# Kernel optimization log

Hardware: AMD Instinct MI355X
Metric: run time of the kernel (lower is better)

The kernel has to match this reference:

```python
import jax, jax.numpy as jnp
import numpy as np

B, I, D = 256, 1152, 8   # batch, input_num_capsule, input_dim_vector
C, O = 10, 16            # num_capsule, dim_vector
NUM_ROUTING = 3
EPS = 1e-7


def squash(s, axis=-1):
    # v = ||s||^2 / (1 + ||s||^2) * s / ||s||
    n2 = jnp.sum(jnp.square(s), axis=axis, keepdims=True)
    return (n2 / (1.0 + n2)) * s / jnp.sqrt(n2 + EPS)


def setup_inputs() -> dict:
    key = jax.random.key(0)
    kx, kw = jax.random.split(key)
    x = jax.random.normal(kx, (B, I, D), dtype=jnp.float32)
    W = jax.random.normal(kw, (I, C, D, O), dtype=jnp.float32) * 0.05
    return {"x": x, "W": W}


def reference(x, W):
    # inputs_hat[b,i,c,o] = sum_d x[b,i,d] * W[i,c,d,o]
    # (the original tf.scan over batch of per-sample batch_dots == this einsum)
    inputs_hat = jnp.einsum('bid,icdo->bico', x, W)  # [B,I,C,O]

    bias = jnp.zeros((1, I, C, 1), dtype=x.dtype)    # routing logits
    outputs = None
    for r in range(NUM_ROUTING):
        c = jax.nn.softmax(bias, axis=2)             # softmax over num_capsule
        s = jnp.sum(c[..., None].squeeze(-1) * inputs_hat, axis=1, keepdims=True)  # [B,1,C,O]
        outputs = squash(s, axis=-1)                 # [B,1,C,O]
        if r != NUM_ROUTING - 1:
            bias = bias + jnp.sum(inputs_hat * outputs, axis=-1, keepdims=False)[..., None].squeeze(-1)[..., None]
    return outputs.reshape(B, C, O)
```

## Files before the change

### kernel.cpp

```cpp
#include <hip/hip_runtime.h>
#include <hip/hip_bf16.h>
#include <math.h>


#define B_ 256
#define I_ 1152
#define D_ 8
#define C_ 10
#define O_ 16
#define CO_ (C_*O_)
#define EPS_ 1e-7f

#define IC1 16
#define NIC1 (I_/IC1)
#define BT 16
#define NBT (B_/BT)
#define T1 320
#define IC3 128
#define NIC3 (I_/IC3)
#define T3 320

__global__ __launch_bounds__(T1) void k1_hat(
    const float* __restrict__ x,
    const float* __restrict__ W,
    __hip_bfloat16* __restrict__ hat,
    float* __restrict__ sPart1)
{
    __shared__ float xs[BT * IC1 * D_];
    __shared__ float sred[BT][CO_];
    const int tid = threadIdx.x;
    const int ic = blockIdx.x, bt = blockIdx.y;
    const int i0 = ic * IC1, b0 = bt * BT;

    for (int j = tid; j < BT * IC1 * D_ / 4; j += T1) {
        const int bb = j >> 5, r = j & 31;
        ((float4*)xs)[j] =
            *(const float4*)&x[(((size_t)(b0 + bb)) * I_ + i0) * D_ + r * 4];
    }
    __syncthreads();

    const int ig = tid / 80, r = tid % 80;
    const int c = r / 8, o2 = r % 8;

    float2 acc[BT];
    #pragma unroll
    for (int bb = 0; bb < BT; ++bb) acc[bb] = make_float2(0.0f, 0.0f);

    const float2* W2 = (const float2*)W;

    for (int k = 0; k < IC1 / 4; ++k) {
        const int il = ig * (IC1 / 4) + k;
        const int i = i0 + il;
        float2 wv[D_];
        const float2* wp = W2 + ((size_t)i * C_ + c) * (D_ * O_ / 2) + o2;
        #pragma unroll
        for (int d = 0; d < D_; ++d) wv[d] = wp[d * (O_ / 2)];
        #pragma unroll
        for (int bb = 0; bb < BT; ++bb) {
            const float* xp = &xs[(bb * IC1 + il) * D_];
            float h0 = 0.0f, h1 = 0.0f;
            #pragma unroll
            for (int d = 0; d < D_; ++d) {
                const float xv = xp[d];
                h0 = fmaf(xv, wv[d].x, h0);
                h1 = fmaf(xv, wv[d].y, h1);
            }
            acc[bb].x += h0; acc[bb].y += h1;
            *(__hip_bfloat162*)&hat[((size_t)(b0 + bb) * I_ + i) * CO_ + c * O_ + o2 * 2] =
                __float22bfloat162_rn(make_float2(h0, h1));
        }
    }

    if (ig == 0) {
        #pragma unroll
        for (int bb = 0; bb < BT; ++bb) {
            sred[bb][c * O_ + o2 * 2]     = acc[bb].x;
            sred[bb][c * O_ + o2 * 2 + 1] = acc[bb].y;
        }
    }
    __syncthreads();
    #pragma unroll
    for (int g = 1; g < 4; ++g) {
        if (ig == g) {
            #pragma unroll
            for (int bb = 0; bb < BT; ++bb) {
                sred[bb][c * O_ + o2 * 2]     += acc[bb].x;
                sred[bb][c * O_ + o2 * 2 + 1] += acc[bb].y;
            }
        }
        __syncthreads();
    }
    if (tid < CO_) {
        for (int bb = 0; bb < BT; ++bb)
            sPart1[((size_t)ic * B_ + (b0 + bb)) * CO_ + tid] = sred[bb][tid];
    }
}

__device__ __forceinline__ void route_body(
    const __hip_bfloat16* __restrict__ hat, const float* vr,
    float* __restrict__ sPartR, int ic, int b, int il, int c, int tid)
{
    __shared__ float pb[32][C_];
    __shared__ float sr[32][CO_ + 4];
    const int i0 = ic * IC3;

    float sacc[O_];
    #pragma unroll
    for (int o = 0; o < O_; ++o) sacc[o] = 0.0f;

    for (int sb = 0; sb < IC3 / 32; ++sb) {
        const int i = i0 + sb * 32 + il;
        const uint4* hp = (const uint4*)&hat[((size_t)b * I_ + i) * CO_ + c * O_];
        const uint4 ha = hp[0], hb = hp[1];
        float hf[O_];
        {
            const unsigned u[8] = {ha.x, ha.y, ha.z, ha.w, hb.x, hb.y, hb.z, hb.w};
            #pragma unroll
            for (int q = 0; q < 8; ++q) {
                hf[2 * q]     = __uint_as_float(u[q] << 16);
                hf[2 * q + 1] = __uint_as_float(u[q] & 0xffff0000u);
            }
        }
        float p = 0.0f;
        #pragma unroll
        for (int o = 0; o < O_; ++o) p = fmaf(hf[o], vr[o], p);
        pb[il][c] = p;
        __syncthreads();
        float pv[C_];
        #pragma unroll
        for (int q = 0; q < C_; ++q) pv[q] = pb[il][q];
        float m = pv[0];
        #pragma unroll
        for (int q = 1; q < C_; ++q) m = fmaxf(m, pv[q]);
        float sum = 0.0f;
        #pragma unroll
        for (int q = 0; q < C_; ++q) sum += __expf(pv[q] - m);
        const float route = __expf(p - m) * __builtin_amdgcn_rcpf(sum);
        #pragma unroll
        for (int o = 0; o < O_; ++o) sacc[o] = fmaf(route, hf[o], sacc[o]);
        __syncthreads();
    }

    #pragma unroll
    for (int o = 0; o < O_; ++o) sr[il][c * O_ + o] = sacc[o];
    __syncthreads();
    if (tid < CO_) {
        float s = 0.0f;
        #pragma unroll
        for (int k = 0; k < 32; ++k) s += sr[k][tid];
        sPartR[((size_t)ic * B_ + b) * CO_ + tid] = s;
    }
}

__global__ __launch_bounds__(T3) void k_route2(
    const __hip_bfloat16* __restrict__ hat,
    const float* __restrict__ veff,
    float* __restrict__ sPartR)
{
    const int tid = threadIdx.x;
    const int il = tid / C_, c = tid % C_;
    const int ic = blockIdx.x, b = blockIdx.y;
    float vr[O_];
    #pragma unroll
    for (int o = 0; o < O_; ++o) vr[o] = veff[(size_t)b * CO_ + c * O_ + o];
    route_body(hat, vr, sPartR, ic, b, il, c, tid);
}

__global__ __launch_bounds__(T3) void k_route3(
    const __hip_bfloat16* __restrict__ hat,
    const float* __restrict__ veff1,
    const float* __restrict__ sPartR1,
    float* __restrict__ sPartR2)
{
    __shared__ float veffs[CO_];
    const int tid = threadIdx.x;
    const int il = tid / C_, c = tid % C_;
    const int ic = blockIdx.x, b = blockIdx.y;

    if (tid < CO_) {
        float s = 0.0f;
        #pragma unroll
        for (int k = 0; k < NIC3; ++k)
            s += sPartR1[((size_t)k * B_ + b) * CO_ + tid];
        float n2 = s * s;
        n2 += __shfl_xor(n2, 1);
        n2 += __shfl_xor(n2, 2);
        n2 += __shfl_xor(n2, 4);
        n2 += __shfl_xor(n2, 8);
        const float sc = n2 / ((1.0f + n2) * sqrtf(n2 + EPS_));
        veffs[tid] = veff1[(size_t)b * CO_ + tid] + s * sc;
    }
    __syncthreads();

    float vr[O_];
    #pragma unroll
    for (int o = 0; o < O_; ++o) vr[o] = veffs[c * O_ + o];
    route_body(hat, vr, sPartR2, ic, b, il, c, tid);
}

__global__ __launch_bounds__(640) void k_squash(
    const float* __restrict__ sPart,
    int nchunk, float scale,
    const float* __restrict__ prev,
    float* __restrict__ dst)
{
    __shared__ float red[4][CO_];
    const int b = blockIdx.x, tid = threadIdx.x;
    const int q = tid / CO_;
    const int co = tid % CO_;
    float s = 0.0f;
    for (int k = q; k < nchunk; k += 4)
        s += sPart[((size_t)k * B_ + b) * CO_ + co];
    red[q][co] = s;
    __syncthreads();
    if (tid < CO_) {
        s = (red[0][co] + red[1][co]) + (red[2][co] + red[3][co]);
        s *= scale;
        float n2 = s * s;
        n2 += __shfl_xor(n2, 1);
        n2 += __shfl_xor(n2, 2);
        n2 += __shfl_xor(n2, 4);
        n2 += __shfl_xor(n2, 8);
        const float sc = n2 / ((1.0f + n2) * sqrtf(n2 + EPS_));
        const float v = s * sc;
        dst[(size_t)b * CO_ + co] = (prev ? prev[(size_t)b * CO_ + co] : 0.0f) + v;
    }
}

#define THREADS 640
#define ILG 8
#define SUBI 4
#define CHUNK (ILG*SUBI)
#define NITER (I_/CHUNK)

__global__ __launch_bounds__(THREADS) void capsule_routing_kernel(
    const float* __restrict__ x, const float* __restrict__ W,
    float* __restrict__ out)
{
    __shared__ float bias[I_ * C_];
    __shared__ float spart[ILG][C_ * O_];
    __shared__ float sv[C_ * O_];
    __shared__ float vv[C_ * O_];
    __shared__ float ech[CHUNK][C_];
    __shared__ float scale[C_];

    const int b   = blockIdx.x;
    const int tid = threadIdx.x;
    for (int j = tid; j < I_ * C_; j += THREADS) bias[j] = 0.0f;
    const int il = tid / 80;
    const int rr = tid % 80;
    const int c  = rr / 8;
    const int o2 = rr % 8;
    const int o0 = o2 * 2;
    const float* xb = x + (size_t)b * I_ * D_;
    const float2* W2 = (const float2*)W;
    __syncthreads();
    {
        float acc0 = 0.0f, acc1 = 0.0f;
        for (int it = 0; it < NITER; ++it) {
            #pragma unroll
            for (int sub = 0; sub < SUBI; ++sub) {
                const int i = it * CHUNK + sub * ILG + il;
                const float* xi = xb + i * D_;
                const float2* wp = W2 + (i * C_ + c) * (D_ * O_ / 2) + o2;
                float h0 = 0.0f, h1 = 0.0f;
                #pragma unroll
                for (int d = 0; d < D_; ++d) {
                    float2 w = wp[d * (O_ / 2)];
                    float xv = xi[d];
                    h0 = fmaf(xv, w.x, h0);
                    h1 = fmaf(xv, w.y, h1);
                }
                acc0 += h0; acc1 += h1;
            }
        }
        spart[il][c * O_ + o0]     = acc0;
        spart[il][c * O_ + o0 + 1] = acc1;
    }
    __syncthreads();
    if (tid < C_ * O_) {
        float s = 0.0f;
        #pragma unroll
        for (int k = 0; k < ILG; ++k) s += spart[k][tid];
        sv[tid] = s * (1.0f / C_);
    }
    __syncthreads();
    if (tid < C_) {
        float n2 = 0.0f;
        #pragma unroll
        for (int o = 0; o < O_; ++o) { float t = sv[tid * O_ + o]; n2 = fmaf(t, t, n2); }
        scale[tid] = n2 / ((1.0f + n2) * sqrtf(n2 + EPS_));
    }
    __syncthreads();
    if (tid < C_ * O_) vv[tid] = sv[tid] * scale[tid / O_];
    __syncthreads();
    for (int pass = 1; pass < 3; ++pass) {
        float sa0 = 0.0f, sa1 = 0.0f;
        for (int it = 0; it < NITER; ++it) {
            float h0s[SUBI], h1s[SUBI];
            const float v0 = vv[c * O_ + o0];
            const float v1 = vv[c * O_ + o0 + 1];
            #pragma unroll
            for (int sub = 0; sub < SUBI; ++sub) {
                const int i = it * CHUNK + sub * ILG + il;
                const float* xi = xb + i * D_;
                const float2* wp = W2 + (i * C_ + c) * (D_ * O_ / 2) + o2;
                float h0 = 0.0f, h1 = 0.0f;
                #pragma unroll
                for (int d = 0; d < D_; ++d) {
                    float2 w = wp[d * (O_ / 2)];
                    float xv = xi[d];
                    h0 = fmaf(xv, w.x, h0);
                    h1 = fmaf(xv, w.y, h1);
                }
                h0s[sub] = h0; h1s[sub] = h1;
                float p = h0 * v0 + h1 * v1;
                p += __shfl_xor(p, 1);
                p += __shfl_xor(p, 2);
                p += __shfl_xor(p, 4);
                if (o2 == 0) bias[i * C_ + c] += p;
            }
            __syncthreads();
            if (tid < CHUNK * C_) {
                const int il2 = tid / C_, cc = tid % C_;
                const int i = it * CHUNK + il2;
                float m = -1e30f;
                #pragma unroll
                for (int k = 0; k < C_; ++k) m = fmaxf(m, bias[i * C_ + k]);
                ech[il2][cc] = __expf(bias[i * C_ + cc] - m);
            }
            __syncthreads();
            #pragma unroll
            for (int sub = 0; sub < SUBI; ++sub) {
                const int icx = sub * ILG + il;
                float sum = 0.0f;
                #pragma unroll
                for (int k = 0; k < C_; ++k) sum += ech[icx][k];
                const float route = ech[icx][c] / sum;
                sa0 = fmaf(route, h0s[sub], sa0);
                sa1 = fmaf(route, h1s[sub], sa1);
            }
            __syncthreads();
        }
        spart[il][c * O_ + o0]     = sa0;
        spart[il][c * O_ + o0 + 1] = sa1;
        __syncthreads();
        if (tid < C_ * O_) {
            float s = 0.0f;
            #pragma unroll
            for (int k = 0; k < ILG; ++k) s += spart[k][tid];
            sv[tid] = s;
        }
        __syncthreads();
        if (tid < C_) {
            float n2 = 0.0f;
            #pragma unroll
            for (int o = 0; o < O_; ++o) { float t = sv[tid * O_ + o]; n2 = fmaf(t, t, n2); }
            scale[tid] = n2 / ((1.0f + n2) * sqrtf(n2 + EPS_));
        }
        __syncthreads();
        if (tid < C_ * O_) vv[tid] = sv[tid] * scale[tid / O_];
        __syncthreads();
    }
    if (tid < C_ * O_) out[(size_t)b * C_ * O_ + tid] = vv[tid];
}

extern "C" void kernel_launch(void* const* d_in, const int* in_sizes, int n_in,
                              void* d_out, int out_size, void* d_ws, size_t ws_size,
                              hipStream_t stream) {
    (void)in_sizes; (void)n_in; (void)out_size;
    const float* x = (const float*)d_in[0];
    const float* W = (const float*)d_in[1];
    float* out = (float*)d_out;

    const size_t hat_b  = (size_t)B_ * I_ * CO_ * sizeof(__hip_bfloat16);
    const size_t sp1_b  = (size_t)NIC1 * B_ * CO_ * sizeof(float);
    const size_t spr_b  = (size_t)NIC3 * B_ * CO_ * sizeof(float);
    const size_t v_b    = (size_t)B_ * CO_ * sizeof(float);
    const size_t need   = hat_b + sp1_b + 2 * spr_b + v_b;

    if (ws_size >= need) {
        char* p = (char*)d_ws;
        __hip_bfloat16* hat = (__hip_bfloat16*)p;  p += hat_b;
        float* sPart1  = (float*)p;                p += sp1_b;
        float* sPartR1 = (float*)p;                p += spr_b;
        float* sPartR2 = (float*)p;                p += spr_b;
        float* veff1   = (float*)p;

        k1_hat<<<dim3(NIC1, NBT), T1, 0, stream>>>(x, W, hat, sPart1);
        k_squash<<<B_, 640, 0, stream>>>(sPart1, NIC1, 1.0f / C_, nullptr, veff1);
        k_route2<<<dim3(NIC3, B_), T3, 0, stream>>>(hat, veff1, sPartR1);
        k_route3<<<dim3(NIC3, B_), T3, 0, stream>>>(hat, veff1, sPartR1, sPartR2);
        k_squash<<<B_, 640, 0, stream>>>(sPartR2, NIC3, 1.0f, nullptr, out);
    } else {
        capsule_routing_kernel<<<B_, THREADS, 0, stream>>>(x, W, out);
    }
}
```

Baseline: 77.02 us.

## Fuse first squash into route2 and double k1 thread count

Removes the separate first squash kernel launch by having every route2 block redundantly reduce the 72 partial sums of the first routing pass and squash them into shared memory. Block 0 of each batch also writes the result out for route3. Separately, k1_hat goes to 640 threads so each thread handles 2 input capsules instead of 4, with an 8-way shared reduction. The fusion saves a launch and a global round trip, but makes each of the 9 route2 blocks per batch read the full sPart1 data again.

```diff
diff --git a/kernel.cpp b/kernel.cpp
--- a/kernel.cpp
+++ b/kernel.cpp
@@ -15,7 +15,7 @@
 #define NIC1 (I_/IC1)
 #define BT 16
 #define NBT (B_/BT)
-#define T1 320
+#define T1 640
 #define IC3 128
 #define NIC3 (I_/IC3)
 #define T3 320
@@ -32,9 +32,9 @@
     const int ic = blockIdx.x, bt = blockIdx.y;
     const int i0 = ic * IC1, b0 = bt * BT;
 
-    for (int j = tid; j < BT * IC1 * D_ / 4; j += T1) {
-        const int bb = j >> 5, r = j & 31;
-        ((float4*)xs)[j] =
+    if (tid < BT * IC1 * D_ / 4) {
+        const int bb = tid >> 5, r = tid & 31;
+        ((float4*)xs)[tid] =
             *(const float4*)&x[(((size_t)(b0 + bb)) * I_ + i0) * D_ + r * 4];
     }
     __syncthreads();
@@ -48,8 +48,9 @@
 
     const float2* W2 = (const float2*)W;
 
-    for (int k = 0; k < IC1 / 4; ++k) {
-        const int il = ig * (IC1 / 4) + k;
+    #pragma unroll
+    for (int k = 0; k < 2; ++k) {
+        const int il = ig * 2 + k;
         const int i = i0 + il;
         float2 wv[D_];
         const float2* wp = W2 + ((size_t)i * C_ + c) * (D_ * O_ / 2) + o2;
@@ -80,7 +81,7 @@
     }
     __syncthreads();
     #pragma unroll
-    for (int g = 1; g < 4; ++g) {
+    for (int g = 1; g < 8; ++g) {
         if (ig == g) {
             #pragma unroll
             for (int bb = 0; bb < BT; ++bb) {
@@ -154,15 +155,43 @@
 
 __global__ __launch_bounds__(T3) void k_route2(
     const __hip_bfloat16* __restrict__ hat,
-    const float* __restrict__ veff,
+    const float* __restrict__ sPart1,
+    float* __restrict__ veff1out,
     float* __restrict__ sPartR)
 {
+    __shared__ float red[2][CO_];
+    __shared__ float veffs[CO_];
     const int tid = threadIdx.x;
     const int il = tid / C_, c = tid % C_;
     const int ic = blockIdx.x, b = blockIdx.y;
+
+    {
+        const int half = tid / CO_;
+        const int co = tid % CO_;
+        float s = 0.0f;
+        #pragma unroll 4
+        for (int k = half * (NIC1 / 2); k < (half + 1) * (NIC1 / 2); ++k)
+            s += sPart1[((size_t)k * B_ + b) * CO_ + co];
+        red[half][co] = s;
+    }
+    __syncthreads();
+    if (tid < CO_) {
+        float s = (red[0][tid] + red[1][tid]) * (1.0f / C_);
+        float n2 = s * s;
+        n2 += __shfl_xor(n2, 1);
+        n2 += __shfl_xor(n2, 2);
+        n2 += __shfl_xor(n2, 4);
+        n2 += __shfl_xor(n2, 8);
+        const float sc = n2 / ((1.0f + n2) * sqrtf(n2 + EPS_));
+        const float v = s * sc;
+        veffs[tid] = v;
+        if (ic == 0) veff1out[(size_t)b * CO_ + tid] = v;
+    }
+    __syncthreads();
+
     float vr[O_];
     #pragma unroll
-    for (int o = 0; o < O_; ++o) vr[o] = veff[(size_t)b * CO_ + c * O_ + o];
+    for (int o = 0; o < O_; ++o) vr[o] = veffs[c * O_ + o];
     route_body(hat, vr, sPartR, ic, b, il, c, tid);
 }
 
@@ -388,8 +417,7 @@
         float* veff1   = (float*)p;
 
         k1_hat<<<dim3(NIC1, NBT), T1, 0, stream>>>(x, W, hat, sPart1);
-        k_squash<<<B_, 640, 0, stream>>>(sPart1, NIC1, 1.0f / C_, nullptr, veff1);
-        k_route2<<<dim3(NIC3, B_), T3, 0, stream>>>(hat, veff1, sPartR1);
+        k_route2<<<dim3(NIC3, B_), T3, 0, stream>>>(hat, sPart1, veff1, sPartR1);
         k_route3<<<dim3(NIC3, B_), T3, 0, stream>>>(hat, veff1, sPartR1, sPartR2);
         k_squash<<<B_, 640, 0, stream>>>(sPartR2, NIC3, 1.0f, nullptr, out);
     } else {
```

Measured after the change: 94.07 us. 1.22x slower.

## Stage hat stores through LDS and fold final squash into last route block

Applied to the files above, without the earlier changes.

In the first kernel, the per-thread 4-byte bf16x2 stores of the intermediate tensor are staged in shared memory and written out as 16-byte uint4 rows, so global writes are contiguous and wide. This adds two block barriers per inner iteration. The final squash kernel launch is removed. Instead, the last block per batch in the third routing kernel, found with an atomic counter reset by the first squash, sums the partials and writes the output. This saves a launch and a dependency gap but adds fences and a serial tail in one block per batch.

```diff
diff --git a/kernel.cpp b/kernel.cpp
--- a/kernel.cpp
+++ b/kernel.cpp
@@ -28,6 +28,7 @@
 {
     __shared__ float xs[BT * IC1 * D_];
     __shared__ float sred[BT][CO_];
+    __shared__ unsigned hst[4 * BT * 80];
     const int tid = threadIdx.x;
     const int ic = blockIdx.x, bt = blockIdx.y;
     const int i0 = ic * IC1, b0 = bt * BT;
@@ -41,6 +42,7 @@
 
     const int ig = tid / 80, r = tid % 80;
     const int c = r / 8, o2 = r % 8;
+    const int rowbb = tid / 20, seg = tid % 20;
 
     float2 acc[BT];
     #pragma unroll
@@ -48,16 +50,15 @@
 
     const float2* W2 = (const float2*)W;
 
-    for (int k = 0; k < IC1 / 4; ++k) {
-        const int il = ig * (IC1 / 4) + k;
-        const int i = i0 + il;
+    for (int k = 0; k < 4; ++k) {
+        const int i = i0 + ig * 4 + k;
         float2 wv[D_];
         const float2* wp = W2 + ((size_t)i * C_ + c) * (D_ * O_ / 2) + o2;
         #pragma unroll
         for (int d = 0; d < D_; ++d) wv[d] = wp[d * (O_ / 2)];
         #pragma unroll
         for (int bb = 0; bb < BT; ++bb) {
-            const float* xp = &xs[(bb * IC1 + il) * D_];
+            const float* xp = &xs[(bb * IC1 + ig * 4 + k) * D_];
             float h0 = 0.0f, h1 = 0.0f;
             #pragma unroll
             for (int d = 0; d < D_; ++d) {
@@ -66,9 +67,16 @@
                 h1 = fmaf(xv, wv[d].y, h1);
             }
             acc[bb].x += h0; acc[bb].y += h1;
-            *(__hip_bfloat162*)&hat[((size_t)(b0 + bb) * I_ + i) * CO_ + c * O_ + o2 * 2] =
-                __float22bfloat162_rn(make_float2(h0, h1));
-        }
+            __hip_bfloat162 pk = __float22bfloat162_rn(make_float2(h0, h1));
+            hst[(ig * BT + bb) * 80 + c * 8 + o2] = *(unsigned*)&pk;
+        }
+        __syncthreads();
+        for (int t = 0; t < 4; ++t) {
+            const int ii = i0 + t * 4 + k;
+            const uint4 v = ((const uint4*)hst)[tid + t * 320];
+            ((uint4*)hat)[((size_t)(b0 + rowbb) * I_ + ii) * 20 + seg] = v;
+        }
+        __syncthreads();
     }
 
     if (ig == 0) {
@@ -170,9 +178,12 @@
     const __hip_bfloat16* __restrict__ hat,
     const float* __restrict__ veff1,
     const float* __restrict__ sPartR1,
-    float* __restrict__ sPartR2)
+    float* __restrict__ sPartR2,
+    int* __restrict__ counter,
+    float* __restrict__ out)
 {
     __shared__ float veffs[CO_];
+    __shared__ int lastflag;
     const int tid = threadIdx.x;
     const int il = tid / C_, c = tid % C_;
     const int ic = blockIdx.x, b = blockIdx.y;
@@ -196,18 +207,44 @@
     #pragma unroll
     for (int o = 0; o < O_; ++o) vr[o] = veffs[c * O_ + o];
     route_body(hat, vr, sPartR2, ic, b, il, c, tid);
+
+    __syncthreads();
+    if (tid == 0) {
+        __threadfence();
+        const int old = atomicAdd(&counter[b], 1);
+        lastflag = (old == NIC3 - 1);
+    }
+    __syncthreads();
+    if (lastflag) {
+        __threadfence();
+        if (tid < CO_) {
+            const volatile float* vp = (const volatile float*)sPartR2;
+            float s = 0.0f;
+            #pragma unroll
+            for (int k = 0; k < NIC3; ++k)
+                s += vp[((size_t)k * B_ + b) * CO_ + tid];
+            float n2 = s * s;
+            n2 += __shfl_xor(n2, 1);
+            n2 += __shfl_xor(n2, 2);
+            n2 += __shfl_xor(n2, 4);
+            n2 += __shfl_xor(n2, 8);
+            const float sc = n2 / ((1.0f + n2) * sqrtf(n2 + EPS_));
+            out[(size_t)b * CO_ + tid] = s * sc;
+        }
+    }
 }
 
 __global__ __launch_bounds__(640) void k_squash(
     const float* __restrict__ sPart,
     int nchunk, float scale,
-    const float* __restrict__ prev,
-    float* __restrict__ dst)
+    float* __restrict__ dst,
+    int* __restrict__ counter)
 {
     __shared__ float red[4][CO_];
     const int b = blockIdx.x, tid = threadIdx.x;
     const int q = tid / CO_;
     const int co = tid % CO_;
+    if (counter && tid == 0) counter[b] = 0;
     float s = 0.0f;
     for (int k = q; k < nchunk; k += 4)
         s += sPart[((size_t)k * B_ + b) * CO_ + co];
@@ -222,8 +259,7 @@
         n2 += __shfl_xor(n2, 4);
         n2 += __shfl_xor(n2, 8);
         const float sc = n2 / ((1.0f + n2) * sqrtf(n2 + EPS_));
-        const float v = s * sc;
-        dst[(size_t)b * CO_ + co] = (prev ? prev[(size_t)b * CO_ + co] : 0.0f) + v;
+        dst[(size_t)b * CO_ + co] = s * sc;
     }
 }
 
@@ -377,7 +413,8 @@
     const size_t sp1_b  = (size_t)NIC1 * B_ * CO_ * sizeof(float);
     const size_t spr_b  = (size_t)NIC3 * B_ * CO_ * sizeof(float);
     const size_t v_b    = (size_t)B_ * CO_ * sizeof(float);
-    const size_t need   = hat_b + sp1_b + 2 * spr_b + v_b;
+    const size_t cnt_b  = (size_t)B_ * sizeof(int);
+    const size_t need   = hat_b + sp1_b + 2 * spr_b + v_b + cnt_b;
 
     if (ws_size >= need) {
         char* p = (char*)d_ws;
@@ -385,13 +422,14 @@
         float* sPart1  = (float*)p;                p += sp1_b;
         float* sPartR1 = (float*)p;                p += spr_b;
         float* sPartR2 = (float*)p;                p += spr_b;
-        float* veff1   = (float*)p;
+        float* veff1   = (float*)p;                p += v_b;
+        int*   counter = (int*)p;
 
         k1_hat<<<dim3(NIC1, NBT), T1, 0, stream>>>(x, W, hat, sPart1);
-        k_squash<<<B_, 640, 0, stream>>>(sPart1, NIC1, 1.0f / C_, nullptr, veff1);
+        k_squash<<<B_, 640, 0, stream>>>(sPart1, NIC1, 1.0f / C_, veff1, counter);
         k_route2<<<dim3(NIC3, B_), T3, 0, stream>>>(hat, veff1, sPartR1);
-        k_route3<<<dim3(NIC3, B_), T3, 0, stream>>>(hat, veff1, sPartR1, sPartR2);
-        k_squash<<<B_, 640, 0, stream>>>(sPartR2, NIC3, 1.0f, nullptr, out);
+        k_route3<<<dim3(NIC3, B_), T3, 0, stream>>>(hat, veff1, sPartR1, sPartR2,
+                                                    counter, out);
     } else {
         capsule_routing_kernel<<<B_, THREADS, 0, stream>>>(x, W, out);
     }
```

New measurement: 271.9 us. 3.53x slower.
